# Performance work log

Hardware: AMD Instinct MI355X
Metric: run time of the kernel (lower is better)

## Reference

```python
import jax, jax.numpy as jnp
import numpy as np

B, N, D, E = 256, 192, 512, 1024
H = E // 2          # MLP hidden = 512
K = 58              # round(0.3 * 192), hardcoded in the torch forward
EPS_L2 = 1e-8
EPS_BN = 1e-5


def setup_inputs() -> dict:
    key = jax.random.key(0)
    ks = jax.random.split(key, 8)
    s = 0.02
    return {
        "all_patch_embeddings": jax.random.normal(ks[0], (B, N, D), dtype=jnp.float32),
        "attention_map": jax.random.uniform(ks[1], (B, N + 1, N + 1), dtype=jnp.float32),
        # fc: Linear(D, E)
        "W_fc": jax.random.normal(ks[2], (E, D), dtype=jnp.float32) * s,
        "b_fc": jnp.zeros((E,), dtype=jnp.float32),
        # mlp layer 0: Linear(D, H) + BatchNorm1d(H) + ReLU
        "W1": jax.random.normal(ks[3], (H, D), dtype=jnp.float32) * s,
        "b1": jnp.zeros((H,), dtype=jnp.float32),
        "gamma1": jnp.ones((H,), dtype=jnp.float32),
        "beta1": jnp.zeros((H,), dtype=jnp.float32),
        # mlp layer 1: Linear(H, E) (no BN/ReLU applied on last layer)
        "W2": jax.random.normal(ks[4], (E, H), dtype=jnp.float32) * s,
        "b2": jnp.zeros((E,), dtype=jnp.float32),
    }


def reference(all_patch_embeddings, attention_map, W_fc, b_fc, W1, b1, gamma1, beta1, W2, b2):
    # CLS-row attention over the 192 patch tokens: [B, N]
    cls_attn = attention_map[:, 0, 1:]
    # torch.sort(descending)[...,:K] == top-k indices (batched, replaces python loop)
    _, idx = jax.lax.top_k(cls_attn, K)                      # [B, K] int32
    # batched gather replacing the per-sample index_select loop
    sel = jnp.take_along_axis(all_patch_embeddings, idx[:, :, None], axis=1)  # [B, K, D]
    # l2norm over last dim
    norm = jnp.sqrt(jnp.sum(sel * sel, axis=-1, keepdims=True)) + EPS_L2
    base = sel / norm
    # .half() cast in the original (round-trip to fp16 precision)
    base = base.astype(jnp.float16).astype(jnp.float32)
    # fc branch
    feat_fc = jnp.einsum('bkd,ed->bke', base, W_fc) + b_fc    # [B, K, E]
    # mlp branch (num_layers=2): Linear -> BN(train-mode batch stats) -> ReLU -> Linear
    h = jnp.einsum('bkd,hd->bkh', base, W1) + b1              # [B, K, H]
    hf = h.reshape(B * K, H)
    mu = jnp.mean(hf, axis=0)
    var = jnp.var(hf, axis=0)
    hf = (hf - mu) * jax.lax.rsqrt(var + EPS_BN) * gamma1 + beta1
    h = jax.nn.relu(hf).reshape(B, K, H)
    feat_mlp = jnp.einsum('bkh,eh->bke', h, W2) + b2          # [B, K, E]
    feats = feat_mlp + feat_fc
    # maxk_pool1d_var with k=1 and lengths == K reduces to max over token dim
    return jnp.max(feats, axis=1).astype(jnp.float32)         # [B, E]
```

## Files before the change

### kernel.cpp

```cpp
#include <hip/hip_runtime.h>
#include <hip/hip_fp16.h>

#define B_ 256
#define N_ 192
#define D_ 512
#define E_ 1024
#define H_ 512
#define K_ 58
#define M_ (B_*K_)
#define M2_ (B_*64)

typedef _Float16 f16;
typedef unsigned int u32;
typedef _Float16 half8 __attribute__((ext_vector_type(8)));
typedef float floatx4 __attribute__((ext_vector_type(4)));

__device__ inline half8 cvt8(float4 f0, float4 f1) {
  half8 r;
  r[0]=(f16)f0.x; r[1]=(f16)f0.y; r[2]=(f16)f0.z; r[3]=(f16)f0.w;
  r[4]=(f16)f1.x; r[5]=(f16)f1.y; r[6]=(f16)f1.z; r[7]=(f16)f1.w;
  return r;
}

__device__ inline void gl_lds16(const f16* g, f16* l) {
  __builtin_amdgcn_global_load_lds((const __attribute__((address_space(1))) u32*)g,
                                   (__attribute__((address_space(3))) u32*)l, 16, 0, 0);
}

__global__ void prep_kernel(const float* __restrict__ Wfc, const float* __restrict__ W2,
                            const float* __restrict__ W1,
                            f16* __restrict__ Wcat, f16* __restrict__ W1_16) {
  int g = blockIdx.x*256 + threadIdx.x;
  if (blockIdx.x < 512) {
    int idx = g*8;
    int e = idx >> 10, c = idx & 1023;
    const float* src = (c < 512) ? (Wfc + (size_t)e*512 + c)
                                 : (W2  + (size_t)e*512 + (c-512));
    half8 o = cvt8(((const float4*)src)[0], ((const float4*)src)[1]);
    *(uint4*)(Wcat + idx) = *(uint4*)&o;
  } else {
    int idx = (g - 512*256)*8;
    const float* src = W1 + idx;
    half8 o = cvt8(((const float4*)src)[0], ((const float4*)src)[1]);
    *(uint4*)(W1_16 + idx) = *(uint4*)&o;
  }
}

__global__ void topk_gather_kernel(const float* __restrict__ attn,
                                   const float* __restrict__ emb,
                                   f16* __restrict__ A16) {
  __shared__ float sv[N_];
  __shared__ int sidx[K_];
  __shared__ int cnt;
  int b = blockIdx.x, t = threadIdx.x;
  if (t == 0) cnt = 0;
  if (t < N_) sv[t] = attn[(size_t)b*193*193 + 1 + t];
  __syncthreads();
  if (t < N_) {
    float v = sv[t]; int rank = 0;
    for (int j = 0; j < N_; ++j) {
      float vj = sv[j];
      rank += (vj > v) || (vj == v && j < t);
    }
    if (rank < K_) sidx[atomicAdd(&cnt, 1)] = t;
  }
  __syncthreads();
  int w = t >> 6, lane = t & 63;
  for (int slot = w; slot < 64; slot += 4) {
    f16* dst = A16 + ((size_t)b*64 + slot)*1024 + lane*8;
    if (slot < K_) {
      const float* src = emb + ((size_t)b*N_ + sidx[slot])*D_ + lane*8;
      float4 v0 = ((const float4*)src)[0];
      float4 v1 = ((const float4*)src)[1];
      float s = v0.x*v0.x + v0.y*v0.y + v0.z*v0.z + v0.w*v0.w
              + v1.x*v1.x + v1.y*v1.y + v1.z*v1.z + v1.w*v1.w;
      #pragma unroll
      for (int off = 32; off > 0; off >>= 1) s += __shfl_xor(s, off);
      float inv = 1.0f / (sqrtf(s) + 1e-8f);
      half8 o;
      o[0]=(f16)(v0.x*inv); o[1]=(f16)(v0.y*inv); o[2]=(f16)(v0.z*inv); o[3]=(f16)(v0.w*inv);
      o[4]=(f16)(v1.x*inv); o[5]=(f16)(v1.y*inv); o[6]=(f16)(v1.z*inv); o[7]=(f16)(v1.w*inv);
      *(uint4*)dst = *(uint4*)&o;
    } else {
      uint4 z; z.x=0u; z.y=0u; z.z=0u; z.w=0u;
      *(uint4*)dst = z;
    }
  }
}

__launch_bounds__(256)
__global__ void gemm1_kernel(const f16* __restrict__ A16, const f16* __restrict__ W1_16,
                             const float* __restrict__ b1, f16* __restrict__ h16,
                             float* __restrict__ csum, float* __restrict__ css) {
  __shared__ f16 sA[128*32];
  __shared__ f16 sB[128*32];
  __shared__ float sSum[4*128];
  __shared__ float sSS[4*128];
  int t = threadIdx.x;
  int m0 = blockIdx.x * 128;
  int n0 = blockIdx.y * 128;
  int lane = t & 63, w = t >> 6, lm = lane & 15, quad = lane >> 4;
  int lrow = lane >> 2, lseg = lane & 3;
  floatx4 acc[2][8] = {};
  const f16* Abase = A16 + (size_t)m0*1024;
  const f16* Bbase = W1_16 + (size_t)n0*512;
  for (int k0 = 0; k0 < 512; k0 += 32) {
    #pragma unroll
    for (int gi = 0; gi < 2; ++gi) {
      int g = w + gi*4;
      gl_lds16(Abase + (size_t)(g*16 + lrow)*1024 + k0 + lseg*8, &sA[g*512]);
      gl_lds16(Bbase + (size_t)(g*16 + lrow)*512  + k0 + lseg*8, &sB[g*512]);
    }
    __syncthreads();
    half8 a0 = *(const half8*)&sA[(w*32      + lm)*32 + quad*8];
    half8 a1 = *(const half8*)&sA[(w*32 + 16 + lm)*32 + quad*8];
    #pragma unroll
    for (int ct = 0; ct < 8; ++ct) {
      half8 bf = *(const half8*)&sB[(ct*16 + lm)*32 + quad*8];
      acc[0][ct] = __builtin_amdgcn_mfma_f32_16x16x32_f16(a0, bf, acc[0][ct], 0, 0, 0);
      acc[1][ct] = __builtin_amdgcn_mfma_f32_16x16x32_f16(a1, bf, acc[1][ct], 0, 0, 0);
    }
    __syncthreads();
  }
  #pragma unroll
  for (int ct = 0; ct < 8; ++ct) {
    int col = n0 + ct*16 + lm;
    float bias = b1[col];
    float s = 0.f, ss = 0.f;
    #pragma unroll
    for (int s2 = 0; s2 < 2; ++s2) {
      int rb = w*32 + s2*16 + quad*4;
      int rib = rb & 63;
      #pragma unroll
      for (int r = 0; r < 4; ++r) {
        float x = acc[s2][ct][r] + bias;
        h16[(size_t)(m0 + rb + r)*H_ + col] = (f16)x;
        if (rib + r < K_) { s += x; ss += x*x; }
      }
    }
    s  += __shfl_xor(s, 16);  s  += __shfl_xor(s, 32);
    ss += __shfl_xor(ss, 16); ss += __shfl_xor(ss, 32);
    if (lane < 16) { sSum[w*128 + ct*16 + lm] = s; sSS[w*128 + ct*16 + lm] = ss; }
  }
  __syncthreads();
  if (t < 128) {
    float s  = sSum[t] + sSum[128+t] + sSum[256+t] + sSum[384+t];
    float ss = sSS[t]  + sSS[128+t]  + sSS[256+t]  + sSS[384+t];
    atomicAdd(&csum[n0 + t], s);
    atomicAdd(&css[n0 + t], ss);
  }
}

__global__ void bnrelu_kernel(const f16* __restrict__ h16, const float* __restrict__ csum,
                              const float* __restrict__ css, const float* __restrict__ gamma,
                              const float* __restrict__ beta, f16* __restrict__ A16) {
  int g = blockIdx.x*256 + threadIdx.x;
  int row = g >> 6;
  int c0 = (g & 63)*8;
  f16* dst = A16 + (size_t)row*1024 + 512 + c0;
  if ((row & 63) >= K_) {
    uint4 z; z.x=0u; z.y=0u; z.z=0u; z.w=0u;
    *(uint4*)dst = z;
    return;
  }
  half8 hv = *(const half8*)(h16 + (size_t)row*512 + c0);
  half8 o;
  #pragma unroll
  for (int i = 0; i < 8; ++i) {
    int j = c0 + i;
    float mu  = csum[j] * (1.0f/M_);
    float var = css[j] * (1.0f/M_) - mu*mu;
    float sc  = gamma[j] * rsqrtf(var + 1e-5f);
    float sh  = beta[j] - mu*sc;
    o[i] = (f16)fmaxf((float)hv[i]*sc + sh, 0.0f);
  }
  *(uint4*)dst = *(uint4*)&o;
}

__launch_bounds__(256)
__global__ void fused_kernel(const f16* __restrict__ A16, const f16* __restrict__ Wcat,
                             const float* __restrict__ bfc, const float* __restrict__ b2,
                             float* __restrict__ out) {
  __shared__ f16 sA[128*32];
  __shared__ f16 sB[128*32];
  __shared__ float sMax[4*128];
  int t = threadIdx.x;
  int e0 = blockIdx.x * 128;
  int lane = t & 63, w = t >> 6, lm = lane & 15, quad = lane >> 4;
  int lrow = lane >> 2, lseg = lane & 3;
  floatx4 acc[2][8] = {};
  const f16* Abase = A16 + (size_t)blockIdx.y*128*1024;
  const f16* Bbase = Wcat + (size_t)e0*1024;
  for (int k0 = 0; k0 < 1024; k0 += 32) {
    #pragma unroll
    for (int gi = 0; gi < 2; ++gi) {
      int g = w + gi*4;
      gl_lds16(Abase + (size_t)(g*16 + lrow)*1024 + k0 + lseg*8, &sA[g*512]);
      gl_lds16(Bbase + (size_t)(g*16 + lrow)*1024 + k0 + lseg*8, &sB[g*512]);
    }
    __syncthreads();
    half8 a0 = *(const half8*)&sA[(w*32      + lm)*32 + quad*8];
    half8 a1 = *(const half8*)&sA[(w*32 + 16 + lm)*32 + quad*8];
    #pragma unroll
    for (int ct = 0; ct < 8; ++ct) {
      half8 bf = *(const half8*)&sB[(ct*16 + lm)*32 + quad*8];
      acc[0][ct] = __builtin_amdgcn_mfma_f32_16x16x32_f16(a0, bf, acc[0][ct], 0, 0, 0);
      acc[1][ct] = __builtin_amdgcn_mfma_f32_16x16x32_f16(a1, bf, acc[1][ct], 0, 0, 0);
    }
    __syncthreads();
  }
  #pragma unroll
  for (int ct = 0; ct < 8; ++ct) {
    float mx = -3.0e38f;
    #pragma unroll
    for (int s2 = 0; s2 < 2; ++s2) {
      int rib = (w*32 + s2*16 + quad*4) & 63;
      #pragma unroll
      for (int r = 0; r < 4; ++r)
        if (rib + r < K_) mx = fmaxf(mx, acc[s2][ct][r]);
    }
    mx = fmaxf(mx, __shfl_xor(mx, 16));
    mx = fmaxf(mx, __shfl_xor(mx, 32));
    if (lane < 16) sMax[w*128 + ct*16 + lm] = mx;
  }
  __syncthreads();
  {
    int bb  = t >> 7;
    int col = t & 127;
    float mx = bb == 0 ? fmaxf(sMax[col], sMax[128+col])
                       : fmaxf(sMax[256+col], sMax[384+col]);
    int e = e0 + col;
    out[((size_t)blockIdx.y*2 + bb)*E_ + e] = mx + bfc[e] + b2[e];
  }
}

extern "C" void kernel_launch(void* const* d_in, const int* in_sizes, int n_in,
                              void* d_out, int out_size, void* d_ws, size_t ws_size,
                              hipStream_t stream) {
  const float* emb   = (const float*)d_in[0];
  const float* attn  = (const float*)d_in[1];
  const float* Wfc   = (const float*)d_in[2];
  const float* bfc   = (const float*)d_in[3];
  const float* W1    = (const float*)d_in[4];
  const float* b1    = (const float*)d_in[5];
  const float* gamma = (const float*)d_in[6];
  const float* beta  = (const float*)d_in[7];
  const float* W2    = (const float*)d_in[8];
  const float* b2    = (const float*)d_in[9];
  float* out = (float*)d_out;

  char* ws = (char*)d_ws;
  f16*   A16   = (f16*)(ws);
  f16*   h16   = (f16*)(ws + 33554432);
  f16*   Wcat  = (f16*)(ws + 50331648);
  f16*   W1_16 = (f16*)(ws + 52428800);
  float* csum  = (float*)(ws + 52953088);
  float* css   = (float*)(ws + 52955136);

  hipMemsetAsync(csum, 0, 4096, stream);

  prep_kernel<<<640, 256, 0, stream>>>(Wfc, W2, W1, Wcat, W1_16);
  topk_gather_kernel<<<B_, 256, 0, stream>>>(attn, emb, A16);
  gemm1_kernel<<<dim3(M2_/128, H_/128), 256, 0, stream>>>(A16, W1_16, b1, h16, csum, css);
  bnrelu_kernel<<<M2_*64/256, 256, 0, stream>>>(h16, csum, css, gamma, beta, A16);
  fused_kernel<<<dim3(E_/128, B_/2), 256, 0, stream>>>(A16, Wcat, bfc, b2, out);
}
```

Before: 271.7 us.

## Merge setup kernels, write GEMM1 output in place, retile GEMMs to 64-row batches

The weight-cast, top-k gather and csum-zeroing steps are merged into one setup kernel, which removes the memset and one launch. GEMM1 now writes its pre-BN output straight into the second half of A16, so the separate h16 buffer is gone and bnrelu works in place. bnrelu precomputes the scale and shift per column into shared memory instead of recomputing them for every element. Both GEMMs move to 64x128 tiles with a K step of 64 (one batch per block), which doubles the block count and drops the wasted max logic across batches, at the cost of less reuse of each loaded B tile.

```diff
diff --git a/kernel.cpp b/kernel.cpp
--- a/kernel.cpp
+++ b/kernel.cpp
@@ -27,98 +27,99 @@
                                    (__attribute__((address_space(3))) u32*)l, 16, 0, 0);
 }
 
-__global__ void prep_kernel(const float* __restrict__ Wfc, const float* __restrict__ W2,
-                            const float* __restrict__ W1,
-                            f16* __restrict__ Wcat, f16* __restrict__ W1_16) {
-  int g = blockIdx.x*256 + threadIdx.x;
-  if (blockIdx.x < 512) {
-    int idx = g*8;
+__global__ void setup_kernel(const float* __restrict__ Wfc, const float* __restrict__ W2,
+                             const float* __restrict__ W1, const float* __restrict__ attn,
+                             const float* __restrict__ emb,
+                             f16* __restrict__ Wcat, f16* __restrict__ W1_16,
+                             f16* __restrict__ A16, float* __restrict__ csum) {
+  __shared__ float sv[N_];
+  __shared__ int sidx[K_];
+  __shared__ int cnt;
+  int blk = blockIdx.x, t = threadIdx.x;
+  if (blk < 512) {
+    int idx = (blk*256 + t)*8;
     int e = idx >> 10, c = idx & 1023;
     const float* src = (c < 512) ? (Wfc + (size_t)e*512 + c)
                                  : (W2  + (size_t)e*512 + (c-512));
     half8 o = cvt8(((const float4*)src)[0], ((const float4*)src)[1]);
     *(uint4*)(Wcat + idx) = *(uint4*)&o;
-  } else {
-    int idx = (g - 512*256)*8;
+  } else if (blk < 640) {
+    int idx = ((blk-512)*256 + t)*8;
     const float* src = W1 + idx;
     half8 o = cvt8(((const float4*)src)[0], ((const float4*)src)[1]);
     *(uint4*)(W1_16 + idx) = *(uint4*)&o;
-  }
-}
-
-__global__ void topk_gather_kernel(const float* __restrict__ attn,
-                                   const float* __restrict__ emb,
-                                   f16* __restrict__ A16) {
-  __shared__ float sv[N_];
-  __shared__ int sidx[K_];
-  __shared__ int cnt;
-  int b = blockIdx.x, t = threadIdx.x;
-  if (t == 0) cnt = 0;
-  if (t < N_) sv[t] = attn[(size_t)b*193*193 + 1 + t];
-  __syncthreads();
-  if (t < N_) {
-    float v = sv[t]; int rank = 0;
-    for (int j = 0; j < N_; ++j) {
-      float vj = sv[j];
-      rank += (vj > v) || (vj == v && j < t);
-    }
-    if (rank < K_) sidx[atomicAdd(&cnt, 1)] = t;
-  }
-  __syncthreads();
-  int w = t >> 6, lane = t & 63;
-  for (int slot = w; slot < 64; slot += 4) {
-    f16* dst = A16 + ((size_t)b*64 + slot)*1024 + lane*8;
-    if (slot < K_) {
-      const float* src = emb + ((size_t)b*N_ + sidx[slot])*D_ + lane*8;
-      float4 v0 = ((const float4*)src)[0];
-      float4 v1 = ((const float4*)src)[1];
-      float s = v0.x*v0.x + v0.y*v0.y + v0.z*v0.z + v0.w*v0.w
-              + v1.x*v1.x + v1.y*v1.y + v1.z*v1.z + v1.w*v1.w;
-      #pragma unroll
-      for (int off = 32; off > 0; off >>= 1) s += __shfl_xor(s, off);
-      float inv = 1.0f / (sqrtf(s) + 1e-8f);
-      half8 o;
-      o[0]=(f16)(v0.x*inv); o[1]=(f16)(v0.y*inv); o[2]=(f16)(v0.z*inv); o[3]=(f16)(v0.w*inv);
-      o[4]=(f16)(v1.x*inv); o[5]=(f16)(v1.y*inv); o[6]=(f16)(v1.z*inv); o[7]=(f16)(v1.w*inv);
-      *(uint4*)dst = *(uint4*)&o;
-    } else {
-      uint4 z; z.x=0u; z.y=0u; z.z=0u; z.w=0u;
-      *(uint4*)dst = z;
-    }
+  } else if (blk < 896) {
+    int b = blk - 640;
+    if (t == 0) cnt = 0;
+    if (t < N_) sv[t] = attn[(size_t)b*193*193 + 1 + t];
+    __syncthreads();
+    if (t < N_) {
+      float v = sv[t]; int rank = 0;
+      for (int j = 0; j < N_; ++j) {
+        float vj = sv[j];
+        rank += (vj > v) || (vj == v && j < t);
+      }
+      if (rank < K_) sidx[atomicAdd(&cnt, 1)] = t;
+    }
+    __syncthreads();
+    int w = t >> 6, lane = t & 63;
+    for (int slot = w; slot < 64; slot += 4) {
+      f16* dst = A16 + ((size_t)b*64 + slot)*1024 + lane*8;
+      if (slot < K_) {
+        const float* src = emb + ((size_t)b*N_ + sidx[slot])*D_ + lane*8;
+        float4 v0 = ((const float4*)src)[0];
+        float4 v1 = ((const float4*)src)[1];
+        float s = v0.x*v0.x + v0.y*v0.y + v0.z*v0.z + v0.w*v0.w
+                + v1.x*v1.x + v1.y*v1.y + v1.z*v1.z + v1.w*v1.w;
+        #pragma unroll
+        for (int off = 32; off > 0; off >>= 1) s += __shfl_xor(s, off);
+        float inv = 1.0f / (sqrtf(s) + 1e-8f);
+        half8 o;
+        o[0]=(f16)(v0.x*inv); o[1]=(f16)(v0.y*inv); o[2]=(f16)(v0.z*inv); o[3]=(f16)(v0.w*inv);
+        o[4]=(f16)(v1.x*inv); o[5]=(f16)(v1.y*inv); o[6]=(f16)(v1.z*inv); o[7]=(f16)(v1.w*inv);
+        *(uint4*)dst = *(uint4*)&o;
+      } else {
+        uint4 z; z.x=0u; z.y=0u; z.z=0u; z.w=0u;
+        *(uint4*)dst = z;
+      }
+    }
+  } else {
+    float4 z; z.x=0.f; z.y=0.f; z.z=0.f; z.w=0.f;
+    ((float4*)csum)[t] = z;
   }
 }
 
 __launch_bounds__(256)
 __global__ void gemm1_kernel(const f16* __restrict__ A16, const f16* __restrict__ W1_16,
-                             const float* __restrict__ b1, f16* __restrict__ h16,
+                             const float* __restrict__ b1, f16* __restrict__ Aout,
                              float* __restrict__ csum, float* __restrict__ css) {
-  __shared__ f16 sA[128*32];
-  __shared__ f16 sB[128*32];
-  __shared__ float sSum[4*128];
-  __shared__ float sSS[4*128];
+  __shared__ f16 sA0[64*32], sA1[64*32];
+  __shared__ f16 sB0[128*32], sB1[128*32];
+  __shared__ float sSum[4*128], sSS[4*128];
   int t = threadIdx.x;
-  int m0 = blockIdx.x * 128;
-  int n0 = blockIdx.y * 128;
+  int n0 = blockIdx.x * 128;
+  int m0 = blockIdx.y * 64;
   int lane = t & 63, w = t >> 6, lm = lane & 15, quad = lane >> 4;
   int lrow = lane >> 2, lseg = lane & 3;
-  floatx4 acc[2][8] = {};
-  const f16* Abase = A16 + (size_t)m0*1024;
-  const f16* Bbase = W1_16 + (size_t)n0*512;
-  for (int k0 = 0; k0 < 512; k0 += 32) {
-    #pragma unroll
-    for (int gi = 0; gi < 2; ++gi) {
-      int g = w + gi*4;
-      gl_lds16(Abase + (size_t)(g*16 + lrow)*1024 + k0 + lseg*8, &sA[g*512]);
-      gl_lds16(Bbase + (size_t)(g*16 + lrow)*512  + k0 + lseg*8, &sB[g*512]);
-    }
-    __syncthreads();
-    half8 a0 = *(const half8*)&sA[(w*32      + lm)*32 + quad*8];
-    half8 a1 = *(const half8*)&sA[(w*32 + 16 + lm)*32 + quad*8];
+  floatx4 acc[8] = {};
+  const f16* Ab = A16 + (size_t)m0*1024;
+  const f16* Bb = W1_16 + (size_t)n0*512;
+  for (int k0 = 0; k0 < 512; k0 += 64) {
+    gl_lds16(Ab + (size_t)(w*16 + lrow)*1024 + k0      + lseg*8, &sA0[w*16*32]);
+    gl_lds16(Ab + (size_t)(w*16 + lrow)*1024 + k0 + 32 + lseg*8, &sA1[w*16*32]);
+    gl_lds16(Bb + (size_t)(w*16 + lrow)*512 + k0      + lseg*8, &sB0[w*16*32]);
+    gl_lds16(Bb + (size_t)(w*16 + lrow)*512 + k0 + 32 + lseg*8, &sB1[w*16*32]);
+    gl_lds16(Bb + (size_t)(64 + w*16 + lrow)*512 + k0      + lseg*8, &sB0[(64 + w*16)*32]);
+    gl_lds16(Bb + (size_t)(64 + w*16 + lrow)*512 + k0 + 32 + lseg*8, &sB1[(64 + w*16)*32]);
+    __syncthreads();
+    half8 a0 = *(const half8*)&sA0[(w*16 + lm)*32 + quad*8];
+    half8 a1 = *(const half8*)&sA1[(w*16 + lm)*32 + quad*8];
     #pragma unroll
     for (int ct = 0; ct < 8; ++ct) {
-      half8 bf = *(const half8*)&sB[(ct*16 + lm)*32 + quad*8];
-      acc[0][ct] = __builtin_amdgcn_mfma_f32_16x16x32_f16(a0, bf, acc[0][ct], 0, 0, 0);
-      acc[1][ct] = __builtin_amdgcn_mfma_f32_16x16x32_f16(a1, bf, acc[1][ct], 0, 0, 0);
+      half8 b0 = *(const half8*)&sB0[(ct*16 + lm)*32 + quad*8];
+      acc[ct] = __builtin_amdgcn_mfma_f32_16x16x32_f16(a0, b0, acc[ct], 0, 0, 0);
+      half8 b1f = *(const half8*)&sB1[(ct*16 + lm)*32 + quad*8];
+      acc[ct] = __builtin_amdgcn_mfma_f32_16x16x32_f16(a1, b1f, acc[ct], 0, 0, 0);
     }
     __syncthreads();
   }
@@ -127,16 +128,12 @@
     int col = n0 + ct*16 + lm;
     float bias = b1[col];
     float s = 0.f, ss = 0.f;
-    #pragma unroll
-    for (int s2 = 0; s2 < 2; ++s2) {
-      int rb = w*32 + s2*16 + quad*4;
-      int rib = rb & 63;
-      #pragma unroll
-      for (int r = 0; r < 4; ++r) {
-        float x = acc[s2][ct][r] + bias;
-        h16[(size_t)(m0 + rb + r)*H_ + col] = (f16)x;
-        if (rib + r < K_) { s += x; ss += x*x; }
-      }
+    int rb = w*16 + quad*4;
+    #pragma unroll
+    for (int r = 0; r < 4; ++r) {
+      float x = acc[ct][r] + bias;
+      Aout[(size_t)(m0 + rb + r)*1024 + 512 + col] = (f16)x;
+      if (rb + r < K_) { s += x; ss += x*x; }
     }
     s  += __shfl_xor(s, 16);  s  += __shfl_xor(s, 32);
     ss += __shfl_xor(ss, 16); ss += __shfl_xor(ss, 32);
@@ -151,86 +148,90 @@
   }
 }
 
-__global__ void bnrelu_kernel(const f16* __restrict__ h16, const float* __restrict__ csum,
+__global__ void bnrelu_kernel(f16* __restrict__ A16, const float* __restrict__ csum,
                               const float* __restrict__ css, const float* __restrict__ gamma,
-                              const float* __restrict__ beta, f16* __restrict__ A16) {
-  int g = blockIdx.x*256 + threadIdx.x;
-  int row = g >> 6;
-  int c0 = (g & 63)*8;
-  f16* dst = A16 + (size_t)row*1024 + 512 + c0;
-  if ((row & 63) >= K_) {
-    uint4 z; z.x=0u; z.y=0u; z.z=0u; z.w=0u;
-    *(uint4*)dst = z;
-    return;
-  }
-  half8 hv = *(const half8*)(h16 + (size_t)row*512 + c0);
-  half8 o;
-  #pragma unroll
-  for (int i = 0; i < 8; ++i) {
-    int j = c0 + i;
+                              const float* __restrict__ beta) {
+  __shared__ float sSc[H_], sSh[H_];
+  int t = threadIdx.x;
+  for (int j = t; j < H_; j += 256) {
     float mu  = csum[j] * (1.0f/M_);
     float var = css[j] * (1.0f/M_) - mu*mu;
     float sc  = gamma[j] * rsqrtf(var + 1e-5f);
-    float sh  = beta[j] - mu*sc;
-    o[i] = (f16)fmaxf((float)hv[i]*sc + sh, 0.0f);
-  }
-  *(uint4*)dst = *(uint4*)&o;
+    sSc[j] = sc;
+    sSh[j] = beta[j] - mu*sc;
+  }
+  __syncthreads();
+  int r0 = blockIdx.x * 16;
+  #pragma unroll
+  for (int i = 0; i < 4; ++i) {
+    int seg = t + 256*i;
+    int row = r0 + (seg >> 6);
+    int c0  = (seg & 63) * 8;
+    f16* p = A16 + (size_t)row*1024 + 512 + c0;
+    if ((row & 63) >= K_) {
+      uint4 z; z.x=0u; z.y=0u; z.z=0u; z.w=0u;
+      *(uint4*)p = z;
+    } else {
+      half8 hv = *(const half8*)p;
+      half8 o;
+      #pragma unroll
+      for (int k = 0; k < 8; ++k)
+        o[k] = (f16)fmaxf((float)hv[k]*sSc[c0+k] + sSh[c0+k], 0.0f);
+      *(uint4*)p = *(uint4*)&o;
+    }
+  }
 }
 
 __launch_bounds__(256)
 __global__ void fused_kernel(const f16* __restrict__ A16, const f16* __restrict__ Wcat,
                              const float* __restrict__ bfc, const float* __restrict__ b2,
                              float* __restrict__ out) {
-  __shared__ f16 sA[128*32];
-  __shared__ f16 sB[128*32];
+  __shared__ f16 sA0[64*32], sA1[64*32];
+  __shared__ f16 sB0[128*32], sB1[128*32];
   __shared__ float sMax[4*128];
   int t = threadIdx.x;
   int e0 = blockIdx.x * 128;
+  int b  = blockIdx.y;
   int lane = t & 63, w = t >> 6, lm = lane & 15, quad = lane >> 4;
   int lrow = lane >> 2, lseg = lane & 3;
-  floatx4 acc[2][8] = {};
-  const f16* Abase = A16 + (size_t)blockIdx.y*128*1024;
-  const f16* Bbase = Wcat + (size_t)e0*1024;
-  for (int k0 = 0; k0 < 1024; k0 += 32) {
-    #pragma unroll
-    for (int gi = 0; gi < 2; ++gi) {
-      int g = w + gi*4;
-      gl_lds16(Abase + (size_t)(g*16 + lrow)*1024 + k0 + lseg*8, &sA[g*512]);
-      gl_lds16(Bbase + (size_t)(g*16 + lrow)*1024 + k0 + lseg*8, &sB[g*512]);
-    }
-    __syncthreads();
-    half8 a0 = *(const half8*)&sA[(w*32      + lm)*32 + quad*8];
-    half8 a1 = *(const half8*)&sA[(w*32 + 16 + lm)*32 + quad*8];
+  floatx4 acc[8] = {};
+  const f16* Ab = A16 + (size_t)b*64*1024;
+  const f16* Bb = Wcat + (size_t)e0*1024;
+  for (int k0 = 0; k0 < 1024; k0 += 64) {
+    gl_lds16(Ab + (size_t)(w*16 + lrow)*1024 + k0      + lseg*8, &sA0[w*16*32]);
+    gl_lds16(Ab + (size_t)(w*16 + lrow)*1024 + k0 + 32 + lseg*8, &sA1[w*16*32]);
+    gl_lds16(Bb + (size_t)(w*16 + lrow)*1024 + k0      + lseg*8, &sB0[w*16*32]);
+    gl_lds16(Bb + (size_t)(w*16 + lrow)*1024 + k0 + 32 + lseg*8, &sB1[w*16*32]);
+    gl_lds16(Bb + (size_t)(64 + w*16 + lrow)*1024 + k0      + lseg*8, &sB0[(64 + w*16)*32]);
+    gl_lds16(Bb + (size_t)(64 + w*16 + lrow)*1024 + k0 + 32 + lseg*8, &sB1[(64 + w*16)*32]);
+    __syncthreads();
+    half8 a0 = *(const half8*)&sA0[(w*16 + lm)*32 + quad*8];
+    half8 a1 = *(const half8*)&sA1[(w*16 + lm)*32 + quad*8];
     #pragma unroll
     for (int ct = 0; ct < 8; ++ct) {
-      half8 bf = *(const half8*)&sB[(ct*16 + lm)*32 + quad*8];
-      acc[0][ct] = __builtin_amdgcn_mfma_f32_16x16x32_f16(a0, bf, acc[0][ct], 0, 0, 0);
-      acc[1][ct] = __builtin_amdgcn_mfma_f32_16x16x32_f16(a1, bf, acc[1][ct], 0, 0, 0);
+      half8 b0 = *(const half8*)&sB0[(ct*16 + lm)*32 + quad*8];
+      acc[ct] = __builtin_amdgcn_mfma_f32_16x16x32_f16(a0, b0, acc[ct], 0, 0, 0);
+      half8 b1f = *(const half8*)&sB1[(ct*16 + lm)*32 + quad*8];
+      acc[ct] = __builtin_amdgcn_mfma_f32_16x16x32_f16(a1, b1f, acc[ct], 0, 0, 0);
     }
     __syncthreads();
   }
   #pragma unroll
   for (int ct = 0; ct < 8; ++ct) {
     float mx = -3.0e38f;
-    #pragma unroll
-    for (int s2 = 0; s2 < 2; ++s2) {
-      int rib = (w*32 + s2*16 + quad*4) & 63;
-      #pragma unroll
-      for (int r = 0; r < 4; ++r)
-        if (rib + r < K_) mx = fmaxf(mx, acc[s2][ct][r]);
-    }
+    int rb = w*16 + quad*4;
+    #pragma unroll
+    for (int r = 0; r < 4; ++r)
+      if (rb + r < K_) mx = fmaxf(mx, acc[ct][r]);
     mx = fmaxf(mx, __shfl_xor(mx, 16));
     mx = fmaxf(mx, __shfl_xor(mx, 32));
     if (lane < 16) sMax[w*128 + ct*16 + lm] = mx;
   }
   __syncthreads();
-  {
-    int bb  = t >> 7;
-    int col = t & 127;
-    float mx = bb == 0 ? fmaxf(sMax[col], sMax[128+col])
-                       : fmaxf(sMax[256+col], sMax[384+col]);
-    int e = e0 + col;
-    out[((size_t)blockIdx.y*2 + bb)*E_ + e] = mx + bfc[e] + b2[e];
+  if (t < 128) {
+    float mx = fmaxf(fmaxf(sMax[t], sMax[128+t]), fmaxf(sMax[256+t], sMax[384+t]));
+    int e = e0 + t;
+    out[(size_t)b*E_ + e] = mx + bfc[e] + b2[e];
   }
 }
 
@@ -251,17 +252,13 @@
 
   char* ws = (char*)d_ws;
   f16*   A16   = (f16*)(ws);
-  f16*   h16   = (f16*)(ws + 33554432);
-  f16*   Wcat  = (f16*)(ws + 50331648);
-  f16*   W1_16 = (f16*)(ws + 52428800);
-  float* csum  = (float*)(ws + 52953088);
-  float* css   = (float*)(ws + 52955136);
-
-  hipMemsetAsync(csum, 0, 4096, stream);
-
-  prep_kernel<<<640, 256, 0, stream>>>(Wfc, W2, W1, Wcat, W1_16);
-  topk_gather_kernel<<<B_, 256, 0, stream>>>(attn, emb, A16);
-  gemm1_kernel<<<dim3(M2_/128, H_/128), 256, 0, stream>>>(A16, W1_16, b1, h16, csum, css);
-  bnrelu_kernel<<<M2_*64/256, 256, 0, stream>>>(h16, csum, css, gamma, beta, A16);
-  fused_kernel<<<dim3(E_/128, B_/2), 256, 0, stream>>>(A16, Wcat, bfc, b2, out);
-}
+  f16*   Wcat  = (f16*)(ws + 33554432);
+  f16*   W1_16 = (f16*)(ws + 35651584);
+  float* csum  = (float*)(ws + 36175872);
+  float* css   = (float*)(ws + 36177920);
+
+  setup_kernel<<<897, 256, 0, stream>>>(Wfc, W2, W1, attn, emb, Wcat, W1_16, A16, csum);
+  gemm1_kernel<<<dim3(H_/128, B_), 256, 0, stream>>>(A16, W1_16, b1, A16, csum, css);
+  bnrelu_kernel<<<M2_/16, 256, 0, stream>>>(A16, csum, css, gamma, beta);
+  fused_kernel<<<dim3(E_/128, B_), 256, 0, stream>>>(A16, Wcat, bfc, b2, out);
+}
```

Result: no change. 266.8 us (-1.8%).
